# Kernel tuning notes

Hardware: AMD Instinct MI355X
Metric: run time of the kernel (lower is better)

The kernel has to match this reference:

```python
import jax, jax.numpy as jnp
import numpy as np

B, D_IN, D_H, D_OUT, D_INT = 1024, 2048, 4096, 2048, 1024


def fwht(x):
    """Fast Walsh-Hadamard transform over a length-2^k vector (unnormalized),
    faithful to the torch chunk/cat butterfly loop."""
    n = x.shape[0]
    k = int(n).bit_length() - 1
    for i in range(k):
        y = x.reshape(2 ** i, 2, -1)        # split butterfly level i
        x = jnp.stack([y[:, 0] + y[:, 1], y[:, 0] - y[:, 1]], axis=1)
    return x.reshape(n)


def fastfood(V, BB, Pi, GG, DD):
    """fastfood_torched: pad -> B*x -> H -> permute -> G* -> H -> slice/scale."""
    LL = BB.shape[0]
    vpad = jnp.zeros((LL,), V.dtype).at[: V.shape[0]].set(V)
    m5 = fwht(fwht(BB * vpad)[Pi] * GG)
    divisor = jnp.sqrt(LL * jnp.sum(GG * GG))
    return m5[:DD] / (divisor * np.sqrt(float(DD) / LL))


def _ff_vars(key, DD):
    LL = 1 << int(np.ceil(np.log2(DD)))
    k1, k2, k3 = jax.random.split(key, 3)
    BB = jnp.where(jax.random.uniform(k1, (LL,)) < 0.5, -1.0, 1.0).astype(jnp.float32)
    Pi = jax.random.permutation(k2, LL).astype(jnp.int32)
    GG = jax.random.normal(k3, (LL,), dtype=jnp.float32)
    return BB, Pi, GG


def setup_inputs():
    key = jax.random.key(0)
    ks = jax.random.split(key, 8)
    x = jax.random.normal(ks[0], (B, D_IN), dtype=jnp.float32)
    V = jax.random.normal(ks[1], (D_INT,), dtype=jnp.float32) * 0.01
    W1_0 = jax.random.normal(ks[2], (D_H, D_IN), dtype=jnp.float32) * 0.02
    b1_0 = jnp.zeros((D_H,), jnp.float32)
    W2_0 = jax.random.normal(ks[3], (D_OUT, D_H), dtype=jnp.float32) * 0.02
    b2_0 = jnp.zeros((D_OUT,), jnp.float32)
    BB_W1, Pi_W1, GG_W1 = _ff_vars(ks[4], D_H * D_IN)
    BB_b1, Pi_b1, GG_b1 = _ff_vars(ks[5], D_H)
    BB_W2, Pi_W2, GG_W2 = _ff_vars(ks[6], D_OUT * D_H)
    BB_b2, Pi_b2, GG_b2 = _ff_vars(ks[7], D_OUT)
    return dict(x=x, V=V, W1_0=W1_0, b1_0=b1_0, W2_0=W2_0, b2_0=b2_0,
                BB_W1=BB_W1, Pi_W1=Pi_W1, GG_W1=GG_W1,
                BB_b1=BB_b1, Pi_b1=Pi_b1, GG_b1=GG_b1,
                BB_W2=BB_W2, Pi_W2=Pi_W2, GG_W2=GG_W2,
                BB_b2=BB_b2, Pi_b2=Pi_b2, GG_b2=GG_b2)


def reference(x, V, W1_0, b1_0, W2_0, b2_0,
              BB_W1, Pi_W1, GG_W1, BB_b1, Pi_b1, GG_b1,
              BB_W2, Pi_W2, GG_W2, BB_b2, Pi_b2, GG_b2):
    # Reconstruct each parameter: theta = theta0 + fastfood(V).view(shape)
    W1 = W1_0 + fastfood(V, BB_W1, Pi_W1, GG_W1, D_H * D_IN).reshape(D_H, D_IN)
    b1 = b1_0 + fastfood(V, BB_b1, Pi_b1, GG_b1, D_H)
    W2 = W2_0 + fastfood(V, BB_W2, Pi_W2, GG_W2, D_OUT * D_H).reshape(D_OUT, D_H)
    b2 = b2_0 + fastfood(V, BB_b2, Pi_b2, GG_b2, D_OUT)
    # Wrapped module forward (2-layer MLP)
    h = jax.nn.relu(x @ W1.T + b1)
    return h @ W2.T + b2
```

## Files before the change

kernel.cpp:

```cpp
#include <hip/hip_runtime.h>
#include <hip/hip_bf16.h>
#include <stdint.h>


typedef __attribute__((ext_vector_type(8))) short bf16x8;
typedef __attribute__((ext_vector_type(8))) short short8;
typedef __attribute__((ext_vector_type(4))) float f32x4;

__device__ __forceinline__ ushort f2bf(float f) {
  union { float f; uint32_t u; } v; v.f = f;
  return (ushort)((v.u + 0x7FFFu + ((v.u >> 16) & 1u)) >> 16);
}
__device__ __forceinline__ float bf2f(ushort u) {
  union { uint32_t u; float f; } v; v.u = (uint32_t)u << 16; return v.f;
}

__device__ __forceinline__ void gload_lds16(const void* g, void* l) {
  __builtin_amdgcn_global_load_lds(
      (const __attribute__((address_space(1))) void*)g,
      (__attribute__((address_space(3))) void*)l, 16, 0, 0);
}

__device__ __forceinline__ void wait_vm16() { asm volatile("s_waitcnt vmcnt(16)" ::: "memory"); }
__device__ __forceinline__ void wait_vm8()  { asm volatile("s_waitcnt vmcnt(8)"  ::: "memory"); }
__device__ __forceinline__ void wait_vm0()  { asm volatile("s_waitcnt vmcnt(0)"  ::: "memory"); }
__device__ __forceinline__ void wait_lgkm0(){ asm volatile("s_waitcnt lgkmcnt(0)" ::: "memory"); }
__device__ __forceinline__ void barrier_raw(){ asm volatile("s_barrier" ::: "memory"); }

template <int NN>
__device__ __forceinline__ void wht_inreg(float* v) {
#pragma unroll
  for (int h = 1; h < NN; h <<= 1)
#pragma unroll
    for (int g = 0; g < NN; g += (h << 1))
#pragma unroll
      for (int k = 0; k < h; ++k) {
        float a = v[g + k], b = v[g + k + h];
        v[g + k] = a + b; v[g + k + h] = a - b;
      }
}

__global__ __launch_bounds__(256) void prep(
    const float4* __restrict__ x4, ushort4* __restrict__ xb4,
    const float* __restrict__ V,
    const float* __restrict__ BBW1, const float* __restrict__ BBW2,
    float* __restrict__ t1, float* __restrict__ t2,
    const float* __restrict__ BBb1, const int* __restrict__ Pib1,
    const float* __restrict__ GGb1, const float* __restrict__ b10,
    const float* __restrict__ BBb2, const int* __restrict__ Pib2,
    const float* __restrict__ GGb2, const float* __restrict__ b20,
    float* __restrict__ ob1, float* __restrict__ ob2) {
  __shared__ float ts[1024];
  __shared__ float zs[4096];
  __shared__ float red[4];
  const int bid = blockIdx.x;
  const int tid = threadIdx.x;

  if (bid < 2048) {
    int i = bid * 256 + tid;
    float4 v = x4[i];
    ushort4 o;
    o.x = f2bf(v.x); o.y = f2bf(v.y); o.z = f2bf(v.z); o.w = f2bf(v.w);
    xb4[i] = o;
    return;
  }

  if (bid < 2050) {
    const int which = bid - 2048;
    const float* BB = which ? BBW2 : BBW1;
    float* t = which ? t2 : t1;
    for (int i = tid; i < 1024; i += 256) ts[i] = BB[i] * V[i];
    for (int st = 0; st < 10; ++st) {
      int half = 1 << st;
      __syncthreads();
      for (int j = tid; j < 512; j += 256) {
        int p = ((j >> st) << (st + 1)) | (j & (half - 1));
        float a = ts[p], b = ts[p + half];
        ts[p] = a + b; ts[p + half] = a - b;
      }
    }
    __syncthreads();
    for (int i = tid; i < 1024; i += 256) t[i] = ts[i];
    return;
  }

  {
    const int which = bid - 2050;
    const int L = which ? 2048 : 4096;
    const float* BB = which ? BBb2 : BBb1;
    const int* Pi = which ? Pib2 : Pib1;
    const float* GG = which ? GGb2 : GGb1;
    const float* b0 = which ? b20 : b10;
    float* ob = which ? ob2 : ob1;

    for (int i = tid; i < 1024; i += 256) ts[i] = BB[i] * V[i];
    for (int st = 0; st < 10; ++st) {
      int half = 1 << st;
      __syncthreads();
      for (int j = tid; j < 512; j += 256) {
        int p = ((j >> st) << (st + 1)) | (j & (half - 1));
        float a = ts[p], b = ts[p + half];
        ts[p] = a + b; ts[p + half] = a - b;
      }
    }
    __syncthreads();
    float gsum = 0.f;
    for (int i = tid; i < L; i += 256) {
      int pi = Pi[i];
      float g = GG[i];
      gsum += g * g;
      zs[i] = ts[pi & 1023] * g;
    }
    for (int o = 32; o > 0; o >>= 1) gsum += __shfl_down(gsum, o);
    if ((tid & 63) == 0) red[tid >> 6] = gsum;
    __syncthreads();
    float ssum = red[0] + red[1] + red[2] + red[3];
    for (int st = 0; (1 << st) < L; ++st) {
      int half = 1 << st;
      __syncthreads();
      for (int j = tid; j < (L >> 1); j += 256) {
        int p = ((j >> st) << (st + 1)) | (j & (half - 1));
        float a = zs[p], b = zs[p + half];
        zs[p] = a + b; zs[p + half] = a - b;
      }
    }
    __syncthreads();
    float scale = rsqrtf((float)L * ssum);
    for (int i = tid; i < L; i += 256) ob[i] = b0[i] + zs[i] * scale;
  }
}

__global__ __launch_bounds__(256) void ff_pass1(
    const int* __restrict__ Pi1, const float* __restrict__ GG1,
    const int* __restrict__ Pi2, const float* __restrict__ GG2,
    const float* __restrict__ t1, const float* __restrict__ t2,
    ushort* __restrict__ inter1, ushort* __restrict__ inter2,
    float* __restrict__ partials) {
  __shared__ float ts[1024];
  __shared__ float zs[8448];
  __shared__ float red[4];
  int tid = threadIdx.x;
  int wsel = blockIdx.x >> 10;
  int blk = blockIdx.x & 1023;
  const int* Pi = wsel ? Pi2 : Pi1;
  const float* GG = wsel ? GG2 : GG1;
  const float* t = wsel ? t2 : t1;
  ushort* inter = wsel ? inter2 : inter1;
  size_t base = (size_t)blk * 8192;

  for (int i = tid; i < 1024; i += 256) ts[i] = t[i];
  __syncthreads();

  const int4* Pi4 = (const int4*)(Pi + base);
  const float4* GG4 = (const float4*)(GG + base);
  float gsum = 0.f;
#pragma unroll
  for (int q = 0; q < 8; ++q) {
    int u = (q << 8) + tid;
    int4 p4 = Pi4[u];
    float4 g4 = GG4[u];
    gsum += g4.x * g4.x + g4.y * g4.y + g4.z * g4.z + g4.w * g4.w;
    int i0 = u << 2;
    float4 z;
    z.x = ts[p4.x & 1023] * g4.x;
    z.y = ts[p4.y & 1023] * g4.y;
    z.z = ts[p4.z & 1023] * g4.z;
    z.w = ts[p4.w & 1023] * g4.w;
    *(float4*)&zs[i0 + (i0 >> 5)] = z;
  }
  for (int o = 32; o > 0; o >>= 1) gsum += __shfl_down(gsum, o);
  if ((tid & 63) == 0) red[tid >> 6] = gsum;
  __syncthreads();
  if (tid == 0) partials[blockIdx.x] = red[0] + red[1] + red[2] + red[3];

  float v[32];
  {
    int o = (tid & 7) | ((tid >> 3) << 8);
#pragma unroll
    for (int r = 0; r < 32; ++r) { int i = o + (r << 3); v[r] = zs[i + (i >> 5)]; }
    wht_inreg<32>(v);
#pragma unroll
    for (int r = 0; r < 32; ++r) { int i = o + (r << 3); zs[i + (i >> 5)] = v[r]; }
  }
  __syncthreads();
  {
#pragma unroll
    for (int r = 0; r < 32; ++r) { int i = tid | (r << 8); v[r] = zs[i + (i >> 5)]; }
    wht_inreg<32>(v);
#pragma unroll
    for (int r = 0; r < 32; ++r) { int i = tid | (r << 8); zs[i + (i >> 5)] = v[r]; }
  }
  __syncthreads();
  {
    int tp = ((tid & 63) << 3) | ((tid >> 6) << 11);
#pragma unroll
    for (int j = 0; j < 4; ++j)
#pragma unroll
      for (int k = 0; k < 8; ++k) { int i = tp + (j << 9) + k; v[(j << 3) + k] = zs[i + (i >> 5)]; }
#pragma unroll
    for (int j = 0; j < 4; ++j) wht_inreg<8>(v + (j << 3));
#pragma unroll
    for (int j = 0; j < 4; ++j) {
      short8 s;
#pragma unroll
      for (int k = 0; k < 8; ++k) s[k] = (short)f2bf(v[(j << 3) + k]);
      *(short8*)(inter + base + tp + (j << 9)) = s;
    }
  }
}

__global__ __launch_bounds__(512) void ff_pass2(
    const ushort* __restrict__ inter1, const ushort* __restrict__ inter2,
    const float* __restrict__ W01, const float* __restrict__ W02,
    const float* __restrict__ partials,
    ushort* __restrict__ W1b, ushort* __restrict__ W2b) {
  __shared__ ushort tile[65536];
  __shared__ float red[8];
  const int tid = threadIdx.x;
  const int wsel = blockIdx.x >> 7;
  const int cb = (blockIdx.x & 127) << 6;
  const ushort* __restrict__ inter = wsel ? inter2 : inter1;
  const float* __restrict__ W0 = wsel ? W02 : W01;
  ushort* __restrict__ Wb = wsel ? W2b : W1b;
  char* tb = (char*)tile;

  float s = partials[(wsel << 10) + tid] + partials[(wsel << 10) + tid + 512];
  for (int o = 32; o > 0; o >>= 1) s += __shfl_down(s, o);
  if ((tid & 63) == 0) red[tid >> 6] = s;

#pragma unroll
  for (int h = 0; h < 2; ++h) {
    int r = tid + (h << 9);
    const ushort* gp = inter + ((size_t)r << 13) + cb;
#pragma unroll
    for (int j = 0; j < 8; ++j) {
      short8 d = *(const short8*)(gp + (j << 3));
      *(short8*)(tb + (r << 7) + ((j ^ (r & 7)) << 4)) = d;
    }
  }
  __syncthreads();
  float ssum = 0.f;
#pragma unroll
  for (int k = 0; k < 8; ++k) ssum += red[k];
  const float sc = rsqrtf(8388608.f * ssum);

  const int p = tid & 31;
  const int j0 = p >> 2;
  const int ob = (p & 3) << 2;
#pragma unroll
  for (int swp = 0; swp < 2; ++swp) {
    const int ge = (tid >> 5) + (swp << 4);
    float va[32], vb[32];
#pragma unroll
    for (int r = 0; r < 32; ++r) {
      int row = (ge << 5) + r;
      ushort2 u = *(const ushort2*)(tb + (row << 7) + ((j0 ^ (row & 7)) << 4) + ob);
      va[r] = bf2f(u.x); vb[r] = bf2f(u.y);
    }
    wht_inreg<32>(va); wht_inreg<32>(vb);
#pragma unroll
    for (int r = 0; r < 32; ++r) {
      int row = (ge << 5) + r;
      ushort2 u; u.x = f2bf(va[r]); u.y = f2bf(vb[r]);
      *(ushort2*)(tb + (row << 7) + ((j0 ^ (row & 7)) << 4) + ob) = u;
    }
  }
  __syncthreads();
#pragma unroll
  for (int swp = 0; swp < 2; ++swp) {
    const int ge = (tid >> 5) + (swp << 4);
    float va[32], vb[32];
#pragma unroll
    for (int r = 0; r < 32; ++r) {
      int row = ge + (r << 5);
      ushort2 u = *(const ushort2*)(tb + (row << 7) + ((j0 ^ (row & 7)) << 4) + ob);
      va[r] = bf2f(u.x); vb[r] = bf2f(u.y);
    }
    wht_inreg<32>(va); wht_inreg<32>(vb);
#pragma unroll
    for (int r = 0; r < 32; ++r) {
      int row = ge + (r << 5);
      ushort2 u; u.x = f2bf(va[r]); u.y = f2bf(vb[r]);
      *(ushort2*)(tb + (row << 7) + ((j0 ^ (row & 7)) << 4) + ob) = u;
    }
  }
  __syncthreads();
#pragma unroll
  for (int h = 0; h < 2; ++h) {
    int r = tid + (h << 9);
    size_t gb = ((size_t)r << 13) + cb;
#pragma unroll
    for (int j = 0; j < 8; ++j) {
      short8 d = *(const short8*)(tb + (r << 7) + ((j ^ (r & 7)) << 4));
      float4 w0a = *(const float4*)(W0 + gb + (j << 3));
      float4 w0b = *(const float4*)(W0 + gb + (j << 3) + 4);
      short8 o;
      o[0] = (short)f2bf(bf2f((ushort)d[0]) * sc + w0a.x);
      o[1] = (short)f2bf(bf2f((ushort)d[1]) * sc + w0a.y);
      o[2] = (short)f2bf(bf2f((ushort)d[2]) * sc + w0a.z);
      o[3] = (short)f2bf(bf2f((ushort)d[3]) * sc + w0a.w);
      o[4] = (short)f2bf(bf2f((ushort)d[4]) * sc + w0b.x);
      o[5] = (short)f2bf(bf2f((ushort)d[5]) * sc + w0b.y);
      o[6] = (short)f2bf(bf2f((ushort)d[6]) * sc + w0b.z);
      o[7] = (short)f2bf(bf2f((ushort)d[7]) * sc + w0b.w);
      *(short8*)(Wb + gb + (j << 3)) = o;
    }
  }
}

template <int EPI, int NT>
__global__ __launch_bounds__(256) void gemm_bt(
    const ushort* __restrict__ A, const ushort* __restrict__ B,
    const float* __restrict__ bias, ushort* __restrict__ Cb, float* __restrict__ Cf,
    int M, int N, int K) {
  __shared__ ushort As[4][8192];
  __shared__ ushort Bs[4][8192];
  const int tid = threadIdx.x;
  const int w = tid >> 6, l = tid & 63;
  const int wr = w >> 1, wc = w & 1;
  const int brow = blockIdx.y << 7, bcol = blockIdx.x << 7;
  const int lrow = l >> 3;
  const int csrc = ((l & 7) ^ lrow) << 3;
  const int l15 = l & 15;
  const int x7 = l15 & 7;
  const int kb = blockIdx.z * (NT << 6);
  f32x4 acc[4][4] = {};

  const ushort* pa = A + (size_t)(brow + (w << 5) + lrow) * K + kb + csrc;
  const ushort* pb = B + (size_t)(bcol + (w << 5) + lrow) * K + kb + csrc;
  const size_t K8 = (size_t)K << 3;

#define STAGE(buf, tt)                                                      \
  {                                                                         \
    const ushort* qa = pa + ((tt) << 6);                                    \
    const ushort* qb = pb + ((tt) << 6);                                    \
    _Pragma("unroll")                                                       \
    for (int i = 0; i < 4; ++i) {                                           \
      gload_lds16(qa + K8 * i, &As[buf][(((w << 2) + i) << 9)]);            \
      gload_lds16(qb + K8 * i, &Bs[buf][(((w << 2) + i) << 9)]);            \
    }                                                                       \
  }

  STAGE(0, 0); STAGE(1, 1); STAGE(2, 2);
  for (int t = 0; t < NT; ++t) {
    if (t < NT - 2) wait_vm16();
    else if (t == NT - 2) wait_vm8();
    else wait_vm0();
    barrier_raw();
    if (t + 3 < NT) STAGE((t + 3) & 3, t + 3);
    const ushort* Acur = As[t & 3];
    const ushort* Bcur = Bs[t & 3];
    bf16x8 af[2][4], bfr[2][4];
#pragma unroll
    for (int kk = 0; kk < 2; ++kk) {
      int c8 = (kk << 2) + (l >> 4);
#pragma unroll
      for (int m = 0; m < 4; ++m)
        af[kk][m] = *(const bf16x8*)&Acur[(((wr << 6) + (m << 4) + l15) << 6) + ((c8 ^ x7) << 3)];
#pragma unroll
      for (int n = 0; n < 4; ++n)
        bfr[kk][n] = *(const bf16x8*)&Bcur[(((wc << 6) + (n << 4) + l15) << 6) + ((c8 ^ x7) << 3)];
    }
    wait_lgkm0();
#pragma unroll
    for (int kk = 0; kk < 2; ++kk)
#pragma unroll
      for (int m = 0; m < 4; ++m)
#pragma unroll
        for (int n = 0; n < 4; ++n)
          acc[m][n] = __builtin_amdgcn_mfma_f32_16x16x32_bf16(af[kk][m], bfr[kk][n], acc[m][n], 0, 0, 0);
  }
#undef STAGE

  if (EPI == 0) {
#pragma unroll
    for (int n = 0; n < 4; ++n) {
      int col = bcol + (wc << 6) + (n << 4) + l15;
      float bv = bias[col];
#pragma unroll
      for (int m = 0; m < 4; ++m) {
        int row0 = brow + (wr << 6) + (m << 4) + ((l >> 4) << 2);
#pragma unroll
        for (int j = 0; j < 4; ++j) {
          float vv = fmaxf(acc[m][n][j] + bv, 0.f);
          Cb[(size_t)(row0 + j) * N + col] = f2bf(vv);
        }
      }
    }
  } else {
    float* outp = Cf + (size_t)blockIdx.z * M * N;
#pragma unroll
    for (int n = 0; n < 4; ++n) {
      int col = bcol + (wc << 6) + (n << 4) + l15;
#pragma unroll
      for (int m = 0; m < 4; ++m) {
        int row0 = brow + (wr << 6) + (m << 4) + ((l >> 4) << 2);
#pragma unroll
        for (int j = 0; j < 4; ++j)
          outp[(size_t)(row0 + j) * N + col] = acc[m][n][j];
      }
    }
  }
}

__global__ __launch_bounds__(256) void reduce_out(
    const float4* __restrict__ P, const float* __restrict__ b2,
    float4* __restrict__ out) {
  int i = blockIdx.x * 256 + threadIdx.x;
  float4 a = P[i], b = P[i + 524288];
  const float4 bb = *(const float4*)(b2 + ((i & 511) << 2));
  float4 o;
  o.x = a.x + b.x + bb.x; o.y = a.y + b.y + bb.y;
  o.z = a.z + b.z + bb.z; o.w = a.w + b.w + bb.w;
  out[i] = o;
}

extern "C" void kernel_launch(void* const* d_in, const int* in_sizes, int n_in,
                              void* d_out, int out_size, void* d_ws, size_t ws_size,
                              hipStream_t stream) {
  const float* x     = (const float*)d_in[0];
  const float* V     = (const float*)d_in[1];
  const float* W1_0  = (const float*)d_in[2];
  const float* b1_0  = (const float*)d_in[3];
  const float* W2_0  = (const float*)d_in[4];
  const float* b2_0  = (const float*)d_in[5];
  const float* BB_W1 = (const float*)d_in[6];
  const int*   Pi_W1 = (const int*)d_in[7];
  const float* GG_W1 = (const float*)d_in[8];
  const float* BB_b1 = (const float*)d_in[9];
  const int*   Pi_b1 = (const int*)d_in[10];
  const float* GG_b1 = (const float*)d_in[11];
  const float* BB_W2 = (const float*)d_in[12];
  const int*   Pi_W2 = (const int*)d_in[13];
  const float* GG_W2 = (const float*)d_in[14];
  const float* BB_b2 = (const float*)d_in[15];
  const int*   Pi_b2 = (const int*)d_in[16];
  const float* GG_b2 = (const float*)d_in[17];
  float* out = (float*)d_out;

  const size_t MB = 1048576ull;
  char* ws = (char*)d_ws;
  ushort* inter1 = (ushort*)(ws);
  float*  P      = (float*)(ws);
  ushort* inter2 = (ushort*)(ws + 16 * MB);
  ushort* W1b    = (ushort*)(ws + 32 * MB);
  ushort* W2b    = (ushort*)(ws + 48 * MB);
  ushort* xb     = (ushort*)(ws + 64 * MB);
  ushort* hb     = (ushort*)(ws + 68 * MB);
  char*   S      = ws + 76 * MB;
  float*  t1     = (float*)(S);
  float*  t2     = (float*)(S + 4096);
  float*  b1     = (float*)(S + 8192);
  float*  b2     = (float*)(S + 8192 + 16384);
  float*  parts  = (float*)(S + 8192 + 16384 + 8192);

  prep<<<2052, 256, 0, stream>>>((const float4*)x, (ushort4*)xb, V,
                                 BB_W1, BB_W2, t1, t2,
                                 BB_b1, Pi_b1, GG_b1, b1_0,
                                 BB_b2, Pi_b2, GG_b2, b2_0, b1, b2);

  ff_pass1<<<2048, 256, 0, stream>>>(Pi_W1, GG_W1, Pi_W2, GG_W2, t1, t2,
                                     inter1, inter2, parts);
  ff_pass2<<<256, 512, 0, stream>>>(inter1, inter2, W1_0, W2_0, parts, W1b, W2b);

  gemm_bt<0, 32><<<dim3(32, 8, 1), 256, 0, stream>>>(xb, W1b, b1, hb, nullptr, 1024, 4096, 2048);
  gemm_bt<1, 32><<<dim3(16, 8, 2), 256, 0, stream>>>(hb, W2b, nullptr, nullptr, P, 1024, 2048, 4096);
  reduce_out<<<2048, 256, 0, stream>>>((const float4*)P, b2, (float4*)out);
}
```

Measured before the change: 171.5 us.

## Split-K both GEMMs with bf16 partials and double-buffered LDS pipeline

Both GEMMs now use split-K: the first splits 2 ways and the second 4 ways, so the grid has more blocks to fill the CUs. Partial results are stored as bf16 instead of fp32, which halves the partial traffic. A separate kernel applies bias and ReLU for layer 1, and a 4-way reduce produces the output. The LDS pipeline drops from 4-stage to 2-stage with a full vmcnt(0) wait, which cuts LDS use but exposes more load latency. Rounding the partials to bf16 costs accuracy, and the extra hfuse launch adds a memory pass.

```diff
diff --git a/kernel.cpp b/kernel.cpp
--- a/kernel.cpp
+++ b/kernel.cpp
@@ -21,8 +21,6 @@
       (__attribute__((address_space(3))) void*)l, 16, 0, 0);
 }
 
-__device__ __forceinline__ void wait_vm16() { asm volatile("s_waitcnt vmcnt(16)" ::: "memory"); }
-__device__ __forceinline__ void wait_vm8()  { asm volatile("s_waitcnt vmcnt(8)"  ::: "memory"); }
 __device__ __forceinline__ void wait_vm0()  { asm volatile("s_waitcnt vmcnt(0)"  ::: "memory"); }
 __device__ __forceinline__ void wait_lgkm0(){ asm volatile("s_waitcnt lgkmcnt(0)" ::: "memory"); }
 __device__ __forceinline__ void barrier_raw(){ asm volatile("s_barrier" ::: "memory"); }
@@ -308,13 +306,14 @@
   }
 }
 
-template <int EPI, int NT>
-__global__ __launch_bounds__(256) void gemm_bt(
+template <int NT>
+__global__ __launch_bounds__(256) void gemm_sp(
     const ushort* __restrict__ A, const ushort* __restrict__ B,
-    const float* __restrict__ bias, ushort* __restrict__ Cb, float* __restrict__ Cf,
+    ushort* __restrict__ P0, ushort* __restrict__ P1,
+    ushort* __restrict__ P2, ushort* __restrict__ P3,
     int M, int N, int K) {
-  __shared__ ushort As[4][8192];
-  __shared__ ushort Bs[4][8192];
+  __shared__ ushort As[2][8192];
+  __shared__ ushort Bs[2][8192];
   const int tid = threadIdx.x;
   const int w = tid >> 6, l = tid & 63;
   const int wr = w >> 1, wc = w & 1;
@@ -323,7 +322,9 @@
   const int csrc = ((l & 7) ^ lrow) << 3;
   const int l15 = l & 15;
   const int x7 = l15 & 7;
-  const int kb = blockIdx.z * (NT << 6);
+  const int z = blockIdx.z;
+  const int kb = z * (NT << 6);
+  ushort* __restrict__ P = z == 0 ? P0 : z == 1 ? P1 : z == 2 ? P2 : P3;
   f32x4 acc[4][4] = {};
 
   const ushort* pa = A + (size_t)(brow + (w << 5) + lrow) * K + kb + csrc;
@@ -341,15 +342,13 @@
     }                                                                       \
   }
 
-  STAGE(0, 0); STAGE(1, 1); STAGE(2, 2);
+  STAGE(0, 0);
   for (int t = 0; t < NT; ++t) {
-    if (t < NT - 2) wait_vm16();
-    else if (t == NT - 2) wait_vm8();
-    else wait_vm0();
+    wait_vm0();
     barrier_raw();
-    if (t + 3 < NT) STAGE((t + 3) & 3, t + 3);
-    const ushort* Acur = As[t & 3];
-    const ushort* Bcur = Bs[t & 3];
+    if (t + 1 < NT) STAGE((t + 1) & 1, t + 1);
+    const ushort* Acur = As[t & 1];
+    const ushort* Bcur = Bs[t & 1];
     bf16x8 af[2][4], bfr[2][4];
 #pragma unroll
     for (int kk = 0; kk < 2; ++kk) {
@@ -372,46 +371,45 @@
   }
 #undef STAGE
 
-  if (EPI == 0) {
-#pragma unroll
-    for (int n = 0; n < 4; ++n) {
-      int col = bcol + (wc << 6) + (n << 4) + l15;
-      float bv = bias[col];
-#pragma unroll
-      for (int m = 0; m < 4; ++m) {
-        int row0 = brow + (wr << 6) + (m << 4) + ((l >> 4) << 2);
-#pragma unroll
-        for (int j = 0; j < 4; ++j) {
-          float vv = fmaxf(acc[m][n][j] + bv, 0.f);
-          Cb[(size_t)(row0 + j) * N + col] = f2bf(vv);
-        }
-      }
-    }
-  } else {
-    float* outp = Cf + (size_t)blockIdx.z * M * N;
-#pragma unroll
-    for (int n = 0; n < 4; ++n) {
-      int col = bcol + (wc << 6) + (n << 4) + l15;
-#pragma unroll
-      for (int m = 0; m < 4; ++m) {
-        int row0 = brow + (wr << 6) + (m << 4) + ((l >> 4) << 2);
-#pragma unroll
-        for (int j = 0; j < 4; ++j)
-          outp[(size_t)(row0 + j) * N + col] = acc[m][n][j];
-      }
-    }
-  }
-}
-
-__global__ __launch_bounds__(256) void reduce_out(
-    const float4* __restrict__ P, const float* __restrict__ b2,
-    float4* __restrict__ out) {
+#pragma unroll
+  for (int n = 0; n < 4; ++n) {
+    int col = bcol + (wc << 6) + (n << 4) + l15;
+#pragma unroll
+    for (int m = 0; m < 4; ++m) {
+      int row0 = brow + (wr << 6) + (m << 4) + ((l >> 4) << 2);
+#pragma unroll
+      for (int j = 0; j < 4; ++j)
+        P[(size_t)(row0 + j) * N + col] = f2bf(acc[m][n][j]);
+    }
+  }
+}
+
+__global__ __launch_bounds__(256) void hfuse(
+    const ushort4* __restrict__ G0, const ushort4* __restrict__ G1,
+    const float* __restrict__ b1, ushort4* __restrict__ hb) {
   int i = blockIdx.x * 256 + threadIdx.x;
-  float4 a = P[i], b = P[i + 524288];
+  ushort4 a = G0[i], b = G1[i];
+  const float4 bv = *(const float4*)(b1 + ((i & 1023) << 2));
+  ushort4 o;
+  o.x = f2bf(fmaxf(bf2f(a.x) + bf2f(b.x) + bv.x, 0.f));
+  o.y = f2bf(fmaxf(bf2f(a.y) + bf2f(b.y) + bv.y, 0.f));
+  o.z = f2bf(fmaxf(bf2f(a.z) + bf2f(b.z) + bv.z, 0.f));
+  o.w = f2bf(fmaxf(bf2f(a.w) + bf2f(b.w) + bv.w, 0.f));
+  hb[i] = o;
+}
+
+__global__ __launch_bounds__(256) void reduce_out4(
+    const ushort4* __restrict__ Q0, const ushort4* __restrict__ Q1,
+    const ushort4* __restrict__ Q2, const ushort4* __restrict__ Q3,
+    const float* __restrict__ b2, float4* __restrict__ out) {
+  int i = blockIdx.x * 256 + threadIdx.x;
+  ushort4 a = Q0[i], b = Q1[i], c = Q2[i], d = Q3[i];
   const float4 bb = *(const float4*)(b2 + ((i & 511) << 2));
   float4 o;
-  o.x = a.x + b.x + bb.x; o.y = a.y + b.y + bb.y;
-  o.z = a.z + b.z + bb.z; o.w = a.w + b.w + bb.w;
+  o.x = bf2f(a.x) + bf2f(b.x) + bf2f(c.x) + bf2f(d.x) + bb.x;
+  o.y = bf2f(a.y) + bf2f(b.y) + bf2f(c.y) + bf2f(d.y) + bb.y;
+  o.z = bf2f(a.z) + bf2f(b.z) + bf2f(c.z) + bf2f(d.z) + bb.z;
+  o.w = bf2f(a.w) + bf2f(b.w) + bf2f(c.w) + bf2f(d.w) + bb.w;
   out[i] = o;
 }
 
@@ -441,8 +439,13 @@
   const size_t MB = 1048576ull;
   char* ws = (char*)d_ws;
   ushort* inter1 = (ushort*)(ws);
-  float*  P      = (float*)(ws);
+  ushort* G0     = (ushort*)(ws);
+  ushort* G1     = (ushort*)(ws + 8 * MB);
   ushort* inter2 = (ushort*)(ws + 16 * MB);
+  ushort* Q0     = (ushort*)(ws + 16 * MB);
+  ushort* Q1     = (ushort*)(ws + 20 * MB);
+  ushort* Q2     = (ushort*)(ws + 24 * MB);
+  ushort* Q3     = (ushort*)(ws + 28 * MB);
   ushort* W1b    = (ushort*)(ws + 32 * MB);
   ushort* W2b    = (ushort*)(ws + 48 * MB);
   ushort* xb     = (ushort*)(ws + 64 * MB);
@@ -463,7 +466,13 @@
                                      inter1, inter2, parts);
   ff_pass2<<<256, 512, 0, stream>>>(inter1, inter2, W1_0, W2_0, parts, W1b, W2b);
 
-  gemm_bt<0, 32><<<dim3(32, 8, 1), 256, 0, stream>>>(xb, W1b, b1, hb, nullptr, 1024, 4096, 2048);
-  gemm_bt<1, 32><<<dim3(16, 8, 2), 256, 0, stream>>>(hb, W2b, nullptr, nullptr, P, 1024, 2048, 4096);
-  reduce_out<<<2048, 256, 0, stream>>>((const float4*)P, b2, (float4*)out);
-}
+  gemm_sp<16><<<dim3(32, 8, 2), 256, 0, stream>>>(xb, W1b, G0, G1, nullptr, nullptr,
+                                                  1024, 4096, 2048);
+  hfuse<<<4096, 256, 0, stream>>>((const ushort4*)G0, (const ushort4*)G1, b1,
+                                  (ushort4*)hb);
+  gemm_sp<16><<<dim3(16, 8, 4), 256, 0, stream>>>(hb, W2b, Q0, Q1, Q2, Q3,
+                                                  1024, 2048, 4096);
+  reduce_out4<<<2048, 256, 0, stream>>>((const ushort4*)Q0, (const ushort4*)Q1,
+                                        (const ushort4*)Q2, (const ushort4*)Q3,
+                                        b2, (float4*)out);
+}
```

After: 157.6 us. 8.1% less time.
